# Optimization experiments

Measured on AMD Instinct MI355X. Metric: run time of the kernel, lower is better.

## Reference

```python
import jax, jax.numpy as jnp
import numpy as np

W_CHAMFER = 1.0
W_SMOOTH = 0.5
K_NEIGHBORS = 8


def _pairwise_sqdist(a, b):
    # a: [B,N,3], b: [B,M,3] -> [B,N,M] squared euclidean distances
    a2 = jnp.sum(a * a, axis=-1)  # [B,N]
    b2 = jnp.sum(b * b, axis=-1)  # [B,M]
    ab = jnp.einsum('bnd,bmd->bnm', a, b)  # [B,N,M]
    d2 = a2[:, :, None] + b2[:, None, :] - 2.0 * ab
    return jnp.maximum(d2, 0.0)


def _chamfer(pc1, pc2):
    d = jnp.sqrt(_pairwise_sqdist(pc1, pc2))  # [B,N,M] euclidean (matches torch.norm)
    d1 = jnp.min(d, axis=2)  # [B,N]
    d2 = jnp.min(d, axis=1)  # [B,M]
    return jnp.mean(d1) + jnp.mean(d2)


def _smoothness(pc, flow, k=K_NEIGHBORS):
    d2 = _pairwise_sqdist(pc, pc)  # [B,N,N]
    # k+1 nearest (squared dist preserves ordering); drop self (index 0)
    _, idx = jax.lax.top_k(-d2, k + 1)  # [B,N,k+1]
    idx = idx[:, :, 1:]  # [B,N,k]
    neighbor_flow = jax.vmap(lambda f, i: f[i])(flow, idx)  # [B,N,k,3]
    diff = flow[:, :, None, :] - neighbor_flow
    return jnp.mean(jnp.linalg.norm(diff, axis=-1))


def setup_inputs() -> dict:
    key = jax.random.key(0)
    k1, k2, k3 = jax.random.split(key, 3)
    B, N, M = 2, 8192, 8192
    pc1 = jax.random.normal(k1, (B, N, 3), dtype=jnp.float32)
    pc2 = jax.random.normal(k2, (B, M, 3), dtype=jnp.float32)
    pred_flow = jax.random.normal(k3, (B, N, 3), dtype=jnp.float32) * 0.1
    return {"pc1": pc1, "pc2": pc2, "pred_flow": pred_flow}


def reference(pc1, pc2, pred_flow):
    pc1_warped = pc1 + pred_flow
    l_chamfer = _chamfer(pc1_warped, pc2)
    l_smooth = _smoothness(pc1, pred_flow)
    return W_CHAMFER * l_chamfer + W_SMOOTH * l_smooth
```

## Files before the change

kernel.cpp:

```cpp
#include <hip/hip_runtime.h>

#define N_PTS 8192
#define BATCH 2
#define KNN 8
#define STILE 2048
#define PPB 16
#define CH_R 8
#define CH_SLICE 256
#define NSLICE (N_PTS / CH_SLICE)
#define CH_BLOCKS 512
#define SM_BLOCKS (N_PTS / PPB * BATCH)
#define WS_STORE_NEED (4 * 1024 * 1024)
#define OFF_MINS 0

__device__ __forceinline__ void ce(unsigned &x, unsigned &y) {
    unsigned lo = min(x, y), hi = max(x, y); x = lo; y = hi;
}

__device__ __forceinline__ void insert4(unsigned o[4], unsigned key) {
    unsigned n0 = min(o[0], key);
    unsigned n1 = max(o[0], min(o[1], key));
    unsigned n2 = max(o[1], min(o[2], key));
    unsigned n3 = max(o[2], min(o[3], key));
    o[0]=n0; o[1]=n1; o[2]=n2; o[3]=n3;
}

__device__ __forceinline__ void merge_stage8(unsigned m[8], int d) {
    unsigned p[8], c[8];
    #pragma unroll
    for (int k = 0; k < 8; ++k) p[k] = __shfl_xor(m[k], d, 64);
    #pragma unroll
    for (int k = 0; k < 8; ++k) c[k] = min(m[k], p[7-k]);
    ce(c[0],c[4]); ce(c[1],c[5]); ce(c[2],c[6]); ce(c[3],c[7]);
    ce(c[0],c[2]); ce(c[1],c[3]); ce(c[4],c[6]); ce(c[5],c[7]);
    ce(c[0],c[1]); ce(c[2],c[3]); ce(c[4],c[5]); ce(c[6],c[7]);
    #pragma unroll
    for (int k = 0; k < 8; ++k) m[k] = c[k];
}

__device__ __forceinline__ void merge64(unsigned m[8]) {
    merge_stage8(m, 1); merge_stage8(m, 2); merge_stage8(m, 4);
    merge_stage8(m, 8); merge_stage8(m, 16); merge_stage8(m, 32);
}

__global__ __launch_bounds__(256, 4) void mega_kernel(
        const float* __restrict__ pc1, const float* __restrict__ pc2,
        const float* __restrict__ flow, float* __restrict__ part,
        unsigned* __restrict__ mins, float* __restrict__ out, int store_mode) {
    __shared__ float4 sq[STILE];
    const int tid = threadIdx.x;
    const int bx = blockIdx.x;

    if (bx < CH_BLOCKS) {
        const int rt    = bx & 3;
        const int slice = (bx >> 2) & 31;
        const int z     = bx >> 7;
        const int b = z & 1, dir = z >> 1;
        const float* P1 = pc1  + (size_t)b * N_PTS * 3;
        const float* P2 = pc2  + (size_t)b * N_PTS * 3;
        const float* FL = flow + (size_t)b * N_PTS * 3;
        const int m0 = slice * CH_SLICE;

        float* sraw = (float*)(sq + 256);
        if (tid < CH_SLICE * 3 / 4) {
            float4 v;
            if (dir == 0) {
                v = ((const float4*)(P2 + (size_t)m0 * 3))[tid];
            } else {
                float4 a = ((const float4*)(P1 + (size_t)m0 * 3))[tid];
                float4 f = ((const float4*)(FL + (size_t)m0 * 3))[tid];
                v = make_float4(a.x + f.x, a.y + f.y, a.z + f.z, a.w + f.w);
            }
            ((float4*)sraw)[tid] = v;
        }

        const int i0 = rt * (256 * CH_R) + tid * CH_R;
        float mx[CH_R], my_[CH_R], mz_[CH_R], p2[CH_R], best[CH_R];
        #pragma unroll
        for (int r = 0; r < CH_R; ++r) {
            int row = i0 + r;
            float px, py, pz;
            if (dir == 0) {
                px = P1[row*3+0] + FL[row*3+0];
                py = P1[row*3+1] + FL[row*3+1];
                pz = P1[row*3+2] + FL[row*3+2];
            } else {
                px = P2[row*3+0]; py = P2[row*3+1]; pz = P2[row*3+2];
            }
            mx[r] = -2.0f * px; my_[r] = -2.0f * py; mz_[r] = -2.0f * pz;
            p2[r] = fmaf(px, px, fmaf(py, py, pz * pz));
            best[r] = __builtin_inff();
        }
        __syncthreads();
        {
            float qx = sraw[tid*3+0], qy = sraw[tid*3+1], qz = sraw[tid*3+2];
            sq[tid] = make_float4(qx, qy, qz, fmaf(qx, qx, fmaf(qy, qy, qz * qz)));
        }
        __syncthreads();

        #pragma unroll 8
        for (int jj = 0; jj < CH_SLICE; ++jj) {
            float4 q = sq[jj];
            #pragma unroll
            for (int r = 0; r < CH_R; ++r) {
                float s = fmaf(mx[r], q.x, fmaf(my_[r], q.y, fmaf(mz_[r], q.z, q.w)));
                best[r] = fminf(best[r], s);
            }
        }

        float d2v[CH_R];
        #pragma unroll
        for (int r = 0; r < CH_R; ++r) d2v[r] = fmaxf(best[r] + p2[r], 0.0f);
        if (store_mode) {
            float* dst = part + ((size_t)(z * NSLICE + slice)) * N_PTS + i0;
            *(float4*)(dst)     = make_float4(d2v[0], d2v[1], d2v[2], d2v[3]);
            *(float4*)(dst + 4) = make_float4(d2v[4], d2v[5], d2v[6], d2v[7]);
        } else {
            #pragma unroll
            for (int r = 0; r < CH_R; ++r)
                atomicMin(&mins[z * N_PTS + i0 + r], __float_as_uint(d2v[r]));
        }
    } else {
        const int s  = bx - CH_BLOCKS;
        const int b  = s >> 9;
        const int sx = s & 511;
        const int wv = tid >> 6, lane = tid & 63;
        const int i0w = sx * PPB + wv * 4;
        const float* P = pc1  + (size_t)b * N_PTS * 3;
        const float* F = flow + (size_t)b * N_PTS * 3;

        float mx[4], my[4], mz[4], p2[4], gr[4];
        unsigned thr[4];
        #pragma unroll
        for (int r = 0; r < 4; ++r) {
            int i = i0w + r;
            float px = P[i*3+0], py = P[i*3+1], pz = P[i*3+2];
            mx[r] = -2.0f * px; my[r] = -2.0f * py; mz[r] = -2.0f * pz;
            p2[r] = fmaf(px, px, fmaf(py, py, pz * pz));
            gr[r] = __builtin_inff();
            thr[r] = 0xFFFFFFFFu;
        }

        unsigned o[4][4];
        #pragma unroll
        for (int r = 0; r < 4; ++r)
            #pragma unroll
            for (int k = 0; k < 4; ++k) o[r][k] = 0xFFFFFFFFu;

        __shared__ float psum[4];

        #pragma unroll 1
        for (int tile = 0; tile < N_PTS / STILE; ++tile) {
            const int t0 = tile * STILE;
            __syncthreads();
            #pragma unroll
            for (int u = tid; u < STILE; u += 256) {
                int g = t0 + u;
                float qx = P[g*3+0], qy = P[g*3+1], qz = P[g*3+2];
                sq[u] = make_float4(qx, qy, qz, fmaf(qx, qx, fmaf(qy, qy, qz * qz)));
            }
            __syncthreads();

            if (tile == 0) {
                #pragma unroll 4
                for (int st = 0; st < STILE / 64; ++st) {
                    float4 qa = sq[st * 64 + lane];
                    int j = st * 64 + lane;
                    #pragma unroll
                    for (int r = 0; r < 4; ++r) {
                        float ss = fmaf(mx[r], qa.x, fmaf(my[r], qa.y, fmaf(mz[r], qa.z, qa.w)));
                        float d2 = fmaxf(ss + p2[r], 0.0f);
                        unsigned key = (__float_as_uint(d2) & 0xFFFFE000u) | (unsigned)j;
                        key = (j == i0w + r) ? 0xFFFFFFFFu : key;
                        insert4(o[r], key);
                    }
                }
            } else {
                #pragma unroll 4
                for (int st = 0; st < STILE / 64; ++st) {
                    float4 qa = sq[st * 64 + lane];
                    int j = t0 + st * 64 + lane;
                    float s0 = fmaf(mx[0], qa.x, fmaf(my[0], qa.y, fmaf(mz[0], qa.z, qa.w)));
                    float s1 = fmaf(mx[1], qa.x, fmaf(my[1], qa.y, fmaf(mz[1], qa.z, qa.w)));
                    float s2 = fmaf(mx[2], qa.x, fmaf(my[2], qa.y, fmaf(mz[2], qa.z, qa.w)));
                    float s3 = fmaf(mx[3], qa.x, fmaf(my[3], qa.y, fmaf(mz[3], qa.z, qa.w)));
                    if (__any(s0 <= gr[0])) {
                        float d2 = fmaxf(s0 + p2[0], 0.0f);
                        unsigned key = (__float_as_uint(d2) & 0xFFFFE000u) | (unsigned)j;
                        key = (j == i0w + 0) ? 0xFFFFFFFFu : key;
                        insert4(o[0], key);
                    }
                    if (__any(s1 <= gr[1])) {
                        float d2 = fmaxf(s1 + p2[1], 0.0f);
                        unsigned key = (__float_as_uint(d2) & 0xFFFFE000u) | (unsigned)j;
                        key = (j == i0w + 1) ? 0xFFFFFFFFu : key;
                        insert4(o[1], key);
                    }
                    if (__any(s2 <= gr[2])) {
                        float d2 = fmaxf(s2 + p2[2], 0.0f);
                        unsigned key = (__float_as_uint(d2) & 0xFFFFE000u) | (unsigned)j;
                        key = (j == i0w + 2) ? 0xFFFFFFFFu : key;
                        insert4(o[2], key);
                    }
                    if (__any(s3 <= gr[3])) {
                        float d2 = fmaxf(s3 + p2[3], 0.0f);
                        unsigned key = (__float_as_uint(d2) & 0xFFFFE000u) | (unsigned)j;
                        key = (j == i0w + 3) ? 0xFFFFFFFFu : key;
                        insert4(o[3], key);
                    }
                }
            }

            if (tile <= 2) {
                #pragma unroll
                for (int r = 0; r < 4; ++r) {
                    unsigned a = max(o[r][3], (unsigned)__shfl_xor((int)o[r][3], 1, 64));
                    a = min(a, (unsigned)__shfl_xor((int)a, 2, 64));
                    a = min(a, (unsigned)__shfl_xor((int)a, 4, 64));
                    a = min(a, (unsigned)__shfl_xor((int)a, 8, 64));
                    a = min(a, (unsigned)__shfl_xor((int)a, 16, 64));
                    a = min(a, (unsigned)__shfl_xor((int)a, 32, 64));
                    thr[r] = min(thr[r], a);
                    float thr_up = __uint_as_float((thr[r] & 0xFFFFE000u) + 0x4000u);
                    gr[r] = thr_up - p2[r];
                }
            }
        }

        unsigned fin[4][8];
        #pragma unroll
        for (int r = 0; r < 4; ++r) {
            unsigned m[8] = {o[r][0], o[r][1], o[r][2], o[r][3],
                             0xFFFFFFFFu, 0xFFFFFFFFu, 0xFFFFFFFFu, 0xFFFFFFFFu};
            merge64(m);
            #pragma unroll
            for (int k = 0; k < 8; ++k) fin[r][k] = m[k];
        }

        const int sel = lane & 31;
        unsigned key = fin[0][0];
        #pragma unroll
        for (int rr = 0; rr < 4; ++rr)
            #pragma unroll
            for (int kk = 0; kk < 8; ++kk)
                if (sel == rr * 8 + kk) key = fin[rr][kk];
        const int r = sel >> 3;
        const int i = i0w + r;
        const int j = (int)(key & (N_PTS - 1));
        float dx = F[i*3+0] - F[j*3+0];
        float dy = F[i*3+1] - F[j*3+1];
        float dz = F[i*3+2] - F[j*3+2];
        float sv = sqrtf(fmaf(dx, dx, fmaf(dy, dy, dz * dz)));
        #pragma unroll
        for (int d = 1; d < 64; d <<= 1) sv += __shfl_xor(sv, d, 64);
        if (lane == 0) psum[wv] = sv;
        __syncthreads();
        if (tid == 0) {
            atomicAdd(out, (psum[0] + psum[1] + psum[2] + psum[3]) *
                           (0.25f / ((float)BATCH * N_PTS * KNN)));
        }
    }
}

__global__ void chamfer_reduce_kernel(const unsigned* __restrict__ mins,
                                      const float* __restrict__ part,
                                      float* __restrict__ out, int store_mode) {
    int t = blockIdx.x * 256 + threadIdx.x;
    float v;
    if (store_mode) {
        int c = t >> 13, row = t & (N_PTS - 1);
        const float* p = part + ((size_t)c * NSLICE) * N_PTS + row;
        v = __builtin_inff();
        #pragma unroll 8
        for (int s = 0; s < NSLICE; ++s) v = fminf(v, p[(size_t)s * N_PTS]);
    } else {
        v = __uint_as_float(mins[t]);
    }
    float d = sqrtf(v) * (1.0f / (float)(BATCH * N_PTS));
    #pragma unroll
    for (int off = 32; off > 0; off >>= 1) d += __shfl_down(d, off, 64);
    __shared__ float wsum[4];
    int wid = threadIdx.x >> 6;
    if ((threadIdx.x & 63) == 0) wsum[wid] = d;
    __syncthreads();
    if (threadIdx.x == 0) atomicAdd(out, wsum[0] + wsum[1] + wsum[2] + wsum[3]);
}

extern "C" void kernel_launch(void* const* d_in, const int* in_sizes, int n_in,
                              void* d_out, int out_size, void* d_ws, size_t ws_size,
                              hipStream_t stream) {
    const float* pc1  = (const float*)d_in[0];
    const float* pc2  = (const float*)d_in[1];
    const float* flow = (const float*)d_in[2];
    float* out = (float*)d_out;
    float* part = (float*)d_ws;
    unsigned* mins = (unsigned*)((char*)d_ws + OFF_MINS);

    const int store_mode = (ws_size >= (size_t)WS_STORE_NEED) ? 1 : 0;

    hipMemsetAsync(out, 0, sizeof(float), stream);
    if (!store_mode) {
        hipMemsetAsync(mins, 0xFF, 4u * N_PTS * sizeof(unsigned), stream);
    }

    mega_kernel<<<dim3(CH_BLOCKS + SM_BLOCKS), 256, 0, stream>>>(
        pc1, pc2, flow, part, mins, out, store_mode);

    chamfer_reduce_kernel<<<dim3(2 * BATCH * N_PTS / 256), 256, 0, stream>>>(
        mins, part, out, store_mode);
}
```

Measured before the change: 151.9 us.

## Fuse chamfer reduction into single kernel and widen smoothness rows per wave

Drops the separate chamfer reduce kernel and workspace partials. Each chamfer block now scans all points in shared-memory tiles, splitting a tile between thread pairs, and reduces its sqrt-min directly into the output with one atomic per block. The smoothness path handles 8 query points per wave instead of 4, which halves the block count. It also seeds the pruning threshold after half a tile using a wave-wide top-4 merge, then gates later candidates with it. Costs are more registers per thread and fewer, longer chamfer blocks that could hurt load balance. The smoothness weight moves to a 0.5 factor in place of 0.25 per block.

```diff
diff --git a/kernel.cpp b/kernel.cpp
--- a/kernel.cpp
+++ b/kernel.cpp
@@ -4,14 +4,11 @@
 #define BATCH 2
 #define KNN 8
 #define STILE 2048
-#define PPB 16
-#define CH_R 8
-#define CH_SLICE 256
-#define NSLICE (N_PTS / CH_SLICE)
-#define CH_BLOCKS 512
-#define SM_BLOCKS (N_PTS / PPB * BATCH)
-#define WS_STORE_NEED (4 * 1024 * 1024)
-#define OFF_MINS 0
+#define SM_PPW 8
+#define SM_PPB 32
+#define SM_BLOCKS (BATCH * N_PTS / SM_PPB)
+#define CH_ROWS 256
+#define CH_BLOCKS (4 * N_PTS / CH_ROWS)
 
 __device__ __forceinline__ void ce(unsigned &x, unsigned &y) {
     unsigned lo = min(x, y), hi = max(x, y); x = lo; y = hi;
@@ -28,7 +25,7 @@
 __device__ __forceinline__ void merge_stage8(unsigned m[8], int d) {
     unsigned p[8], c[8];
     #pragma unroll
-    for (int k = 0; k < 8; ++k) p[k] = __shfl_xor(m[k], d, 64);
+    for (int k = 0; k < 8; ++k) p[k] = (unsigned)__shfl_xor((int)m[k], d, 64);
     #pragma unroll
     for (int k = 0; k < 8; ++k) c[k] = min(m[k], p[7-k]);
     ce(c[0],c[4]); ce(c[1],c[5]); ce(c[2],c[6]); ce(c[3],c[7]);
@@ -45,109 +42,75 @@
 
 __global__ __launch_bounds__(256, 4) void mega_kernel(
         const float* __restrict__ pc1, const float* __restrict__ pc2,
-        const float* __restrict__ flow, float* __restrict__ part,
-        unsigned* __restrict__ mins, float* __restrict__ out, int store_mode) {
+        const float* __restrict__ flow, float* __restrict__ out) {
     __shared__ float4 sq[STILE];
+    __shared__ float psum[4];
     const int tid = threadIdx.x;
     const int bx = blockIdx.x;
 
-    if (bx < CH_BLOCKS) {
-        const int rt    = bx & 3;
-        const int slice = (bx >> 2) & 31;
-        const int z     = bx >> 7;
-        const int b = z & 1, dir = z >> 1;
-        const float* P1 = pc1  + (size_t)b * N_PTS * 3;
-        const float* P2 = pc2  + (size_t)b * N_PTS * 3;
-        const float* FL = flow + (size_t)b * N_PTS * 3;
-        const int m0 = slice * CH_SLICE;
-
-        float* sraw = (float*)(sq + 256);
-        if (tid < CH_SLICE * 3 / 4) {
-            float4 v;
-            if (dir == 0) {
-                v = ((const float4*)(P2 + (size_t)m0 * 3))[tid];
-            } else {
-                float4 a = ((const float4*)(P1 + (size_t)m0 * 3))[tid];
-                float4 f = ((const float4*)(FL + (size_t)m0 * 3))[tid];
-                v = make_float4(a.x + f.x, a.y + f.y, a.z + f.z, a.w + f.w);
-            }
-            ((float4*)sraw)[tid] = v;
-        }
-
-        const int i0 = rt * (256 * CH_R) + tid * CH_R;
-        float mx[CH_R], my_[CH_R], mz_[CH_R], p2[CH_R], best[CH_R];
-        #pragma unroll
-        for (int r = 0; r < CH_R; ++r) {
-            int row = i0 + r;
-            float px, py, pz;
-            if (dir == 0) {
-                px = P1[row*3+0] + FL[row*3+0];
-                py = P1[row*3+1] + FL[row*3+1];
-                pz = P1[row*3+2] + FL[row*3+2];
-            } else {
-                px = P2[row*3+0]; py = P2[row*3+1]; pz = P2[row*3+2];
-            }
-            mx[r] = -2.0f * px; my_[r] = -2.0f * py; mz_[r] = -2.0f * pz;
-            p2[r] = fmaf(px, px, fmaf(py, py, pz * pz));
-            best[r] = __builtin_inff();
-        }
-        __syncthreads();
-        {
-            float qx = sraw[tid*3+0], qy = sraw[tid*3+1], qz = sraw[tid*3+2];
-            sq[tid] = make_float4(qx, qy, qz, fmaf(qx, qx, fmaf(qy, qy, qz * qz)));
-        }
-        __syncthreads();
-
-        #pragma unroll 8
-        for (int jj = 0; jj < CH_SLICE; ++jj) {
-            float4 q = sq[jj];
-            #pragma unroll
-            for (int r = 0; r < CH_R; ++r) {
-                float s = fmaf(mx[r], q.x, fmaf(my_[r], q.y, fmaf(mz_[r], q.z, q.w)));
-                best[r] = fminf(best[r], s);
-            }
-        }
-
-        float d2v[CH_R];
-        #pragma unroll
-        for (int r = 0; r < CH_R; ++r) d2v[r] = fmaxf(best[r] + p2[r], 0.0f);
-        if (store_mode) {
-            float* dst = part + ((size_t)(z * NSLICE + slice)) * N_PTS + i0;
-            *(float4*)(dst)     = make_float4(d2v[0], d2v[1], d2v[2], d2v[3]);
-            *(float4*)(dst + 4) = make_float4(d2v[4], d2v[5], d2v[6], d2v[7]);
-        } else {
-            #pragma unroll
-            for (int r = 0; r < CH_R; ++r)
-                atomicMin(&mins[z * N_PTS + i0 + r], __float_as_uint(d2v[r]));
-        }
-    } else {
-        const int s  = bx - CH_BLOCKS;
-        const int b  = s >> 9;
-        const int sx = s & 511;
+    if (bx < SM_BLOCKS) {
+        const int b = bx >> 8, sx = bx & 255;
         const int wv = tid >> 6, lane = tid & 63;
-        const int i0w = sx * PPB + wv * 4;
+        const int i0w = sx * SM_PPB + wv * SM_PPW;
         const float* P = pc1  + (size_t)b * N_PTS * 3;
         const float* F = flow + (size_t)b * N_PTS * 3;
 
-        float mx[4], my[4], mz[4], p2[4], gr[4];
-        unsigned thr[4];
-        #pragma unroll
-        for (int r = 0; r < 4; ++r) {
+        float mx[8], my[8], mz[8], p2[8], gr[8];
+        unsigned thr[8], o[8][4];
+        #pragma unroll
+        for (int r = 0; r < 8; ++r) {
             int i = i0w + r;
             float px = P[i*3+0], py = P[i*3+1], pz = P[i*3+2];
             mx[r] = -2.0f * px; my[r] = -2.0f * py; mz[r] = -2.0f * pz;
             p2[r] = fmaf(px, px, fmaf(py, py, pz * pz));
             gr[r] = __builtin_inff();
             thr[r] = 0xFFFFFFFFu;
-        }
-
-        unsigned o[4][4];
-        #pragma unroll
-        for (int r = 0; r < 4; ++r)
             #pragma unroll
             for (int k = 0; k < 4; ++k) o[r][k] = 0xFFFFFFFFu;
-
-        __shared__ float psum[4];
+        }
+
+        auto update_thr = [&]() {
+            #pragma unroll
+            for (int r = 0; r < 8; ++r) {
+                unsigned m0 = o[r][0], m1 = o[r][1], m2 = o[r][2], m3 = o[r][3];
+                #pragma unroll
+                for (int d = 1; d <= 16; d <<= 1) {
+                    unsigned q0 = (unsigned)__shfl_xor((int)m0, d, 64);
+                    unsigned q1 = (unsigned)__shfl_xor((int)m1, d, 64);
+                    unsigned q2 = (unsigned)__shfl_xor((int)m2, d, 64);
+                    unsigned q3 = (unsigned)__shfl_xor((int)m3, d, 64);
+                    unsigned c0 = min(m0, q3), c1 = min(m1, q2);
+                    unsigned c2 = min(m2, q1), c3 = min(m3, q0);
+                    ce(c0, c2); ce(c1, c3); ce(c0, c1); ce(c2, c3);
+                    m0 = c0; m1 = c1; m2 = c2; m3 = c3;
+                }
+                unsigned bound = max(m3, (unsigned)__shfl_xor((int)m3, 32, 64));
+                thr[r] = min(thr[r], bound);
+                float thr_up = __uint_as_float((thr[r] & 0xFFFFE000u) + 0x4000u);
+                gr[r] = thr_up - p2[r];
+            }
+        };
+
+        auto gated_span = [&](int t0, int st0, int st1) {
+            #pragma unroll 2
+            for (int st = st0; st < st1; ++st) {
+                float4 qa = sq[st * 64 + lane];
+                int j = t0 + st * 64 + lane;
+                float s[8];
+                #pragma unroll
+                for (int r = 0; r < 8; ++r)
+                    s[r] = fmaf(mx[r], qa.x, fmaf(my[r], qa.y, fmaf(mz[r], qa.z, qa.w)));
+                #pragma unroll
+                for (int r = 0; r < 8; ++r) {
+                    if (__any(s[r] <= gr[r])) {
+                        float d2 = fmaxf(s[r] + p2[r], 0.0f);
+                        unsigned key = (__float_as_uint(d2) & 0xFFFFE000u) | (unsigned)j;
+                        key = (j == i0w + r) ? 0xFFFFFFFFu : key;
+                        insert4(o[r], key);
+                    }
+                }
+            }
+        };
 
         #pragma unroll 1
         for (int tile = 0; tile < N_PTS / STILE; ++tile) {
@@ -163,11 +126,11 @@
 
             if (tile == 0) {
                 #pragma unroll 4
-                for (int st = 0; st < STILE / 64; ++st) {
+                for (int st = 0; st < 16; ++st) {
                     float4 qa = sq[st * 64 + lane];
                     int j = st * 64 + lane;
                     #pragma unroll
-                    for (int r = 0; r < 4; ++r) {
+                    for (int r = 0; r < 8; ++r) {
                         float ss = fmaf(mx[r], qa.x, fmaf(my[r], qa.y, fmaf(mz[r], qa.z, qa.w)));
                         float d2 = fmaxf(ss + p2[r], 0.0f);
                         unsigned key = (__float_as_uint(d2) & 0xFFFFE000u) | (unsigned)j;
@@ -175,78 +138,30 @@
                         insert4(o[r], key);
                     }
                 }
+                update_thr();
+                gated_span(0, 16, 32);
             } else {
-                #pragma unroll 4
-                for (int st = 0; st < STILE / 64; ++st) {
-                    float4 qa = sq[st * 64 + lane];
-                    int j = t0 + st * 64 + lane;
-                    float s0 = fmaf(mx[0], qa.x, fmaf(my[0], qa.y, fmaf(mz[0], qa.z, qa.w)));
-                    float s1 = fmaf(mx[1], qa.x, fmaf(my[1], qa.y, fmaf(mz[1], qa.z, qa.w)));
-                    float s2 = fmaf(mx[2], qa.x, fmaf(my[2], qa.y, fmaf(mz[2], qa.z, qa.w)));
-                    float s3 = fmaf(mx[3], qa.x, fmaf(my[3], qa.y, fmaf(mz[3], qa.z, qa.w)));
-                    if (__any(s0 <= gr[0])) {
-                        float d2 = fmaxf(s0 + p2[0], 0.0f);
-                        unsigned key = (__float_as_uint(d2) & 0xFFFFE000u) | (unsigned)j;
-                        key = (j == i0w + 0) ? 0xFFFFFFFFu : key;
-                        insert4(o[0], key);
-                    }
-                    if (__any(s1 <= gr[1])) {
-                        float d2 = fmaxf(s1 + p2[1], 0.0f);
-                        unsigned key = (__float_as_uint(d2) & 0xFFFFE000u) | (unsigned)j;
-                        key = (j == i0w + 1) ? 0xFFFFFFFFu : key;
-                        insert4(o[1], key);
-                    }
-                    if (__any(s2 <= gr[2])) {
-                        float d2 = fmaxf(s2 + p2[2], 0.0f);
-                        unsigned key = (__float_as_uint(d2) & 0xFFFFE000u) | (unsigned)j;
-                        key = (j == i0w + 2) ? 0xFFFFFFFFu : key;
-                        insert4(o[2], key);
-                    }
-                    if (__any(s3 <= gr[3])) {
-                        float d2 = fmaxf(s3 + p2[3], 0.0f);
-                        unsigned key = (__float_as_uint(d2) & 0xFFFFE000u) | (unsigned)j;
-                        key = (j == i0w + 3) ? 0xFFFFFFFFu : key;
-                        insert4(o[3], key);
-                    }
-                }
-            }
-
-            if (tile <= 2) {
-                #pragma unroll
-                for (int r = 0; r < 4; ++r) {
-                    unsigned a = max(o[r][3], (unsigned)__shfl_xor((int)o[r][3], 1, 64));
-                    a = min(a, (unsigned)__shfl_xor((int)a, 2, 64));
-                    a = min(a, (unsigned)__shfl_xor((int)a, 4, 64));
-                    a = min(a, (unsigned)__shfl_xor((int)a, 8, 64));
-                    a = min(a, (unsigned)__shfl_xor((int)a, 16, 64));
-                    a = min(a, (unsigned)__shfl_xor((int)a, 32, 64));
-                    thr[r] = min(thr[r], a);
-                    float thr_up = __uint_as_float((thr[r] & 0xFFFFE000u) + 0x4000u);
-                    gr[r] = thr_up - p2[r];
-                }
-            }
-        }
-
-        unsigned fin[4][8];
-        #pragma unroll
-        for (int r = 0; r < 4; ++r) {
+                gated_span(t0, 0, 32);
+                if (tile == 1) update_thr();
+            }
+        }
+
+        const int pr = lane >> 3, kk = lane & 7;
+        unsigned mykey = 0xFFFFFFFFu;
+        #pragma unroll
+        for (int r = 0; r < 8; ++r) {
             unsigned m[8] = {o[r][0], o[r][1], o[r][2], o[r][3],
                              0xFFFFFFFFu, 0xFFFFFFFFu, 0xFFFFFFFFu, 0xFFFFFFFFu};
             merge64(m);
-            #pragma unroll
-            for (int k = 0; k < 8; ++k) fin[r][k] = m[k];
-        }
-
-        const int sel = lane & 31;
-        unsigned key = fin[0][0];
-        #pragma unroll
-        for (int rr = 0; rr < 4; ++rr)
-            #pragma unroll
-            for (int kk = 0; kk < 8; ++kk)
-                if (sel == rr * 8 + kk) key = fin[rr][kk];
-        const int r = sel >> 3;
-        const int i = i0w + r;
-        const int j = (int)(key & (N_PTS - 1));
+            if (pr == r) {
+                unsigned k2 = m[0];
+                #pragma unroll
+                for (int t = 1; t < 8; ++t) k2 = (kk == t) ? m[t] : k2;
+                mykey = k2;
+            }
+        }
+        const int i = i0w + pr;
+        const int j = (int)(mykey & (N_PTS - 1));
         float dx = F[i*3+0] - F[j*3+0];
         float dy = F[i*3+1] - F[j*3+1];
         float dz = F[i*3+2] - F[j*3+2];
@@ -257,33 +172,89 @@
         __syncthreads();
         if (tid == 0) {
             atomicAdd(out, (psum[0] + psum[1] + psum[2] + psum[3]) *
-                           (0.25f / ((float)BATCH * N_PTS * KNN)));
+                           (0.5f / ((float)BATCH * N_PTS * KNN)));
+        }
+    } else {
+        const int cb = bx - SM_BLOCKS;
+        const int z  = cb >> 5;
+        const int rb = cb & 31;
+        const int b = z & 1, dir = z >> 1;
+        const float* P1 = pc1  + (size_t)b * N_PTS * 3;
+        const float* P2 = pc2  + (size_t)b * N_PTS * 3;
+        const float* FL = flow + (size_t)b * N_PTS * 3;
+        const int wv = tid >> 6, lane = tid & 63;
+        const int rw = tid >> 1, sub = tid & 1;
+        const int r0 = rb * CH_ROWS + rw * 2;
+
+        float mx0, my0, mz0, p20, mx1, my1, mz1, p21;
+        {
+            float px, py, pz;
+            if (dir == 0) {
+                px = P1[r0*3+0] + FL[r0*3+0];
+                py = P1[r0*3+1] + FL[r0*3+1];
+                pz = P1[r0*3+2] + FL[r0*3+2];
+            } else {
+                px = P2[r0*3+0]; py = P2[r0*3+1]; pz = P2[r0*3+2];
+            }
+            mx0 = -2.0f * px; my0 = -2.0f * py; mz0 = -2.0f * pz;
+            p20 = fmaf(px, px, fmaf(py, py, pz * pz));
+            int r1 = r0 + 1;
+            if (dir == 0) {
+                px = P1[r1*3+0] + FL[r1*3+0];
+                py = P1[r1*3+1] + FL[r1*3+1];
+                pz = P1[r1*3+2] + FL[r1*3+2];
+            } else {
+                px = P2[r1*3+0]; py = P2[r1*3+1]; pz = P2[r1*3+2];
+            }
+            mx1 = -2.0f * px; my1 = -2.0f * py; mz1 = -2.0f * pz;
+            p21 = fmaf(px, px, fmaf(py, py, pz * pz));
+        }
+        float b0 = __builtin_inff(), b1 = __builtin_inff();
+
+        #pragma unroll 1
+        for (int tile = 0; tile < N_PTS / STILE; ++tile) {
+            const int t0 = tile * STILE;
+            __syncthreads();
+            #pragma unroll
+            for (int u = tid; u < STILE; u += 256) {
+                int g = t0 + u;
+                float qx, qy, qz;
+                if (dir == 0) {
+                    qx = P2[g*3+0]; qy = P2[g*3+1]; qz = P2[g*3+2];
+                } else {
+                    qx = P1[g*3+0] + FL[g*3+0];
+                    qy = P1[g*3+1] + FL[g*3+1];
+                    qz = P1[g*3+2] + FL[g*3+2];
+                }
+                sq[u] = make_float4(qx, qy, qz, fmaf(qx, qx, fmaf(qy, qy, qz * qz)));
+            }
+            __syncthreads();
+
+            const float4* base = sq + sub * (STILE / 2);
+            #pragma unroll 8
+            for (int c = 0; c < STILE / 2; ++c) {
+                float4 q = base[c];
+                float s0 = fmaf(mx0, q.x, fmaf(my0, q.y, fmaf(mz0, q.z, q.w)));
+                float s1 = fmaf(mx1, q.x, fmaf(my1, q.y, fmaf(mz1, q.z, q.w)));
+                b0 = fminf(b0, s0);
+                b1 = fminf(b1, s1);
+            }
+        }
+
+        b0 = fminf(b0, __shfl_xor(b0, 1, 64));
+        b1 = fminf(b1, __shfl_xor(b1, 1, 64));
+        float val = (sub == 0)
+            ? (sqrtf(fmaxf(b0 + p20, 0.0f)) + sqrtf(fmaxf(b1 + p21, 0.0f)))
+            : 0.0f;
+        #pragma unroll
+        for (int d = 1; d < 64; d <<= 1) val += __shfl_xor(val, d, 64);
+        if (lane == 0) psum[wv] = val;
+        __syncthreads();
+        if (tid == 0) {
+            atomicAdd(out, (psum[0] + psum[1] + psum[2] + psum[3]) *
+                           (1.0f / ((float)BATCH * N_PTS)));
         }
     }
-}
-
-__global__ void chamfer_reduce_kernel(const unsigned* __restrict__ mins,
-                                      const float* __restrict__ part,
-                                      float* __restrict__ out, int store_mode) {
-    int t = blockIdx.x * 256 + threadIdx.x;
-    float v;
-    if (store_mode) {
-        int c = t >> 13, row = t & (N_PTS - 1);
-        const float* p = part + ((size_t)c * NSLICE) * N_PTS + row;
-        v = __builtin_inff();
-        #pragma unroll 8
-        for (int s = 0; s < NSLICE; ++s) v = fminf(v, p[(size_t)s * N_PTS]);
-    } else {
-        v = __uint_as_float(mins[t]);
-    }
-    float d = sqrtf(v) * (1.0f / (float)(BATCH * N_PTS));
-    #pragma unroll
-    for (int off = 32; off > 0; off >>= 1) d += __shfl_down(d, off, 64);
-    __shared__ float wsum[4];
-    int wid = threadIdx.x >> 6;
-    if ((threadIdx.x & 63) == 0) wsum[wid] = d;
-    __syncthreads();
-    if (threadIdx.x == 0) atomicAdd(out, wsum[0] + wsum[1] + wsum[2] + wsum[3]);
 }
 
 extern "C" void kernel_launch(void* const* d_in, const int* in_sizes, int n_in,
@@ -293,19 +264,7 @@
     const float* pc2  = (const float*)d_in[1];
     const float* flow = (const float*)d_in[2];
     float* out = (float*)d_out;
-    float* part = (float*)d_ws;
-    unsigned* mins = (unsigned*)((char*)d_ws + OFF_MINS);
-
-    const int store_mode = (ws_size >= (size_t)WS_STORE_NEED) ? 1 : 0;
 
     hipMemsetAsync(out, 0, sizeof(float), stream);
-    if (!store_mode) {
-        hipMemsetAsync(mins, 0xFF, 4u * N_PTS * sizeof(unsigned), stream);
-    }
-
-    mega_kernel<<<dim3(CH_BLOCKS + SM_BLOCKS), 256, 0, stream>>>(
-        pc1, pc2, flow, part, mins, out, store_mode);
-
-    chamfer_reduce_kernel<<<dim3(2 * BATCH * N_PTS / 256), 256, 0, stream>>>(
-        mins, part, out, store_mode);
-}
+    mega_kernel<<<dim3(SM_BLOCKS + CH_BLOCKS), 256, 0, stream>>>(pc1, pc2, flow, out);
+}
```

Result: slower. 165.7 us (+9.1%).
